# Kernel tuning notes

Measured on AMD Instinct MI355X. Metric: run time of the kernel, lower is better.

The kernel has to match this reference:

```python
import jax, jax.numpy as jnp
import numpy as np

B, N, D, H, DK, DV, R = 4, 256, 256, 8, 32, 32, 64
EPS = 1e-6


def setup_inputs() -> dict:
    key = jax.random.key(0)
    ks = jax.random.split(key, 16)
    s = D ** -0.5
    return {
        "q": jax.random.normal(ks[0], (B, N, D), jnp.float32),
        "k": jax.random.normal(ks[1], (B, N, D), jnp.float32),
        "v": jax.random.normal(ks[2], (B, N, D), jnp.float32),
        "mask": jax.random.randint(ks[3], (B, N, N), 0, 2).astype(jnp.int32),
        "link": jax.random.uniform(ks[4], (B, N, N, R), jnp.float32),
        "Wq": jax.random.normal(ks[5], (D, H * DK), jnp.float32) * s,
        "Wk": jax.random.normal(ks[6], (D, H * DK), jnp.float32) * s,
        "Wr": jax.random.normal(ks[7], (D, H * DK), jnp.float32) * s,
        "Wv": jax.random.normal(ks[8], (D, H * DV), jnp.float32) * s,
        "Wvv": jax.random.normal(ks[9], (D, H * DV), jnp.float32) * s,
        "relationE": jax.random.normal(ks[10], (R, D), jnp.float32) * s,
        "Wo": jax.random.normal(ks[11], (H * DV, D), jnp.float32) * s,
        "gamma": jnp.ones((D,), jnp.float32),
        "beta": jnp.zeros((D,), jnp.float32),
    }


def reference(q, k, v, mask, link, Wq, Wk, Wr, Wv, Wvv, relationE, Wo, gamma, beta):
    # rela_num != 0 branch of Ruleformer MultiHeadAttention (dropout = identity, eval mode).
    residual = q
    b, n, d = q.shape
    # per-head projections of X (== q == residual in this branch): [b,h,n,dk]
    Xq = (q @ Wq).reshape(b, n, H, DK).transpose(0, 2, 1, 3)
    Xk = (q @ Wk).reshape(b, n, H, DK).transpose(0, 2, 1, 3)
    Xv = (q @ Wv).reshape(b, n, H, DV).transpose(0, 2, 1, 3)

    # calcE: relation-biased scores. Rk[b,i,j,h,d] = (link @ relationE @ Wr)
    Rk = jnp.einsum('bijr,re->bije', link, relationE @ Wr).reshape(b, n, n, H, DK)
    # attn[b,h,i,j] = Xq[b,h,i] . (Xk[b,h,j] + Rk[b,i,j,h])
    attn = jnp.einsum('bhid,bhjd->bhij', Xq, Xk)
    attn = attn + jnp.einsum('bijhd,bhid->bhij', Rk, Xq)
    attn = attn / (DK ** 0.5)
    attn = jnp.where(mask[:, None, :, :] == 0, -1e9, attn)
    alpha = jax.nn.softmax(attn, axis=-1)  # [b,h,n,n]

    # calcZ: Z[b,h,i] = sum_j alpha[b,h,i,j] * (Xv[b,h,j] + Rv[b,i,j,h])
    Rv = jnp.einsum('bijr,re->bije', link, relationE @ Wvv).reshape(b, n, n, H, DV)
    Z = jnp.einsum('bhij,bhjd->bhid', alpha, Xv)
    Z = Z + jnp.einsum('bhij,bijhd->bhid', alpha, Rv)

    out = Z.transpose(0, 2, 1, 3).reshape(b, n, H * DV) @ Wo
    out = out + residual
    mu = out.mean(-1, keepdims=True)
    var = ((out - mu) ** 2).mean(-1, keepdims=True)
    out = (out - mu) * jax.lax.rsqrt(var + EPS) * gamma + beta
    return out, alpha
```

## Files before the change

### kernel.cpp

```cpp
#include <hip/hip_runtime.h>
#include <math.h>

constexpr int B_ = 4, N_ = 256, D_ = 256, H_ = 8, DK_ = 32, DV_ = 32, R_ = 64;
constexpr float SCALE_ = 0.17677669529663687f;
constexpr float EPS_ = 1e-6f;

__global__ __launch_bounds__(256) void ekev_kernel(
        const float* __restrict__ relE, const float* __restrict__ Wr,
        const float* __restrict__ Wvv, float* __restrict__ Ek,
        float* __restrict__ Ev) {
    int r = blockIdx.x & 63;
    int which = blockIdx.x >> 6;
    const float* W = which ? Wvv : Wr;
    float* out = which ? Ev : Ek;
    __shared__ float row[256];
    int tid = threadIdx.x;
    row[tid] = relE[r * 256 + tid];
    __syncthreads();
    float acc = 0.f;
    for (int d = 0; d < 256; ++d) acc += row[d] * W[d * 256 + tid];
    out[r * 256 + tid] = acc;
}

__global__ __launch_bounds__(256) void mcat_kernel(
        const float* __restrict__ Wq, const float* __restrict__ Ek,
        float* __restrict__ M) {
    int d = blockIdx.x;
    int t = threadIdx.x;
    __shared__ float wrow[256];
    wrow[t] = Wq[d * 256 + t];
    __syncthreads();
    for (int hr = t; hr < 512; hr += 256) {
        int h = hr >> 6, r = hr & 63;
        const float4* ek4 = (const float4*)(Ek + r * 256 + h * 32);
        const float4* w4 = (const float4*)(wrow + h * 32);
        float acc = 0.f;
#pragma unroll
        for (int k = 0; k < 8; ++k) {
            float4 e = ek4[k], w = w4[k];
            acc += e.x * w.x + e.y * w.y + e.z * w.z + e.w * w.w;
        }
        M[d * 512 + hr] = acc;
    }
}

__global__ __launch_bounds__(256) void projT_kernel(
        const float* __restrict__ q, const float* __restrict__ Wq,
        const float* __restrict__ Wk, const float* __restrict__ Wv,
        const float* __restrict__ M, float* __restrict__ Xq,
        float* __restrict__ Xk, float* __restrict__ Xv,
        float* __restrict__ T) {
    int ct = blockIdx.x >> 4, rt = blockIdx.x & 15;
    int t = threadIdx.x;
    __shared__ float ash[32 * 65];
    __shared__ float bsh[32 * 64];
    const float* W;
    int ncols, cbase;
    if (ct < 4)       { W = Wq; cbase = ct * 64;        ncols = 256; }
    else if (ct < 8)  { W = Wk; cbase = (ct - 4) * 64;  ncols = 256; }
    else if (ct < 12) { W = Wv; cbase = (ct - 8) * 64;  ncols = 256; }
    else              { W = M;  cbase = (ct - 12) * 64; ncols = 512; }
    int ti = t >> 4, tj = t & 15;
    float acc[4][4] = {{0.f}};
    for (int kc = 0; kc < 8; ++kc) {
        __syncthreads();
#pragma unroll
        for (int kk = 0; kk < 2; ++kk) {
            int m = t + kk * 256;
            int i = m >> 3, kq = m & 7;
            float4 v = *(const float4*)(q + (size_t)(rt * 64 + i) * 256 + kc * 32 + kq * 4);
            ash[(kq * 4 + 0) * 65 + i] = v.x;
            ash[(kq * 4 + 1) * 65 + i] = v.y;
            ash[(kq * 4 + 2) * 65 + i] = v.z;
            ash[(kq * 4 + 3) * 65 + i] = v.w;
        }
#pragma unroll
        for (int kk = 0; kk < 2; ++kk) {
            int m = t + kk * 256;
            int k = m >> 4, j4 = m & 15;
            float4 v = *(const float4*)(W + (size_t)(kc * 32 + k) * ncols + cbase + j4 * 4);
            *(float4*)(bsh + k * 64 + j4 * 4) = v;
        }
        __syncthreads();
#pragma unroll 8
        for (int k = 0; k < 32; ++k) {
            float4 av = *(const float4*)(ash + k * 65 + ti * 4);
            float4 bv = *(const float4*)(bsh + k * 64 + tj * 4);
            acc[0][0] += av.x * bv.x; acc[0][1] += av.x * bv.y;
            acc[0][2] += av.x * bv.z; acc[0][3] += av.x * bv.w;
            acc[1][0] += av.y * bv.x; acc[1][1] += av.y * bv.y;
            acc[1][2] += av.y * bv.z; acc[1][3] += av.y * bv.w;
            acc[2][0] += av.z * bv.x; acc[2][1] += av.z * bv.y;
            acc[2][2] += av.z * bv.z; acc[2][3] += av.z * bv.w;
            acc[3][0] += av.w * bv.x; acc[3][1] += av.w * bv.y;
            acc[3][2] += av.w * bv.z; acc[3][3] += av.w * bv.w;
        }
    }
    if (ct < 12) {
        float* dst = (ct < 4) ? Xq : (ct < 8) ? Xk : Xv;
        int gcol = (ct & 3) * 64 + tj * 4;
        int h = gcol >> 5, dk = gcol & 31;
#pragma unroll
        for (int a = 0; a < 4; ++a) {
            int row = rt * 64 + ti * 4 + a;
            int bb = row >> 8, n = row & 255;
            *(float4*)(dst + ((size_t)(bb * 8 + h) * 256 + n) * 32 + dk) =
                make_float4(acc[a][0], acc[a][1], acc[a][2], acc[a][3]);
        }
    } else {
        int gcol = (ct - 12) * 64 + tj * 4;
#pragma unroll
        for (int a = 0; a < 4; ++a) {
            int row = rt * 64 + ti * 4 + a;
            *(float4*)(T + (size_t)row * 512 + gcol) =
                make_float4(acc[a][0], acc[a][1], acc[a][2], acc[a][3]);
        }
    }
}

__global__ __launch_bounds__(256) void qk_kernel(
        const float* __restrict__ Xq, const float* __restrict__ Xk,
        float* __restrict__ qk) {
    int x = blockIdx.x;
    int jt = x & 3, it = (x >> 2) & 3, bh = x >> 4;
    int t = threadIdx.x;
    __shared__ float xqsh[32 * 64];
    __shared__ float xksh[32 * 64];
#pragma unroll
    for (int k = 0; k < 2; ++k) {
        int m = t + k * 256;
        int i = m >> 3, dq4 = m & 7;
        float4 v = *(const float4*)(Xq + ((size_t)(bh * 256 + it * 64 + i)) * 32 + dq4 * 4);
        xqsh[(dq4 * 4 + 0) * 64 + i] = v.x;
        xqsh[(dq4 * 4 + 1) * 64 + i] = v.y;
        xqsh[(dq4 * 4 + 2) * 64 + i] = v.z;
        xqsh[(dq4 * 4 + 3) * 64 + i] = v.w;
        float4 u = *(const float4*)(Xk + ((size_t)(bh * 256 + jt * 64 + i)) * 32 + dq4 * 4);
        xksh[(dq4 * 4 + 0) * 64 + i] = u.x;
        xksh[(dq4 * 4 + 1) * 64 + i] = u.y;
        xksh[(dq4 * 4 + 2) * 64 + i] = u.z;
        xksh[(dq4 * 4 + 3) * 64 + i] = u.w;
    }
    __syncthreads();
    int ti = t >> 4, tj = t & 15;
    float acc[4][4] = {{0.f}};
#pragma unroll 8
    for (int dk = 0; dk < 32; ++dk) {
        float4 av = *(const float4*)(xqsh + dk * 64 + ti * 4);
        float4 bv = *(const float4*)(xksh + dk * 64 + tj * 4);
        acc[0][0] += av.x * bv.x; acc[0][1] += av.x * bv.y;
        acc[0][2] += av.x * bv.z; acc[0][3] += av.x * bv.w;
        acc[1][0] += av.y * bv.x; acc[1][1] += av.y * bv.y;
        acc[1][2] += av.y * bv.z; acc[1][3] += av.y * bv.w;
        acc[2][0] += av.z * bv.x; acc[2][1] += av.z * bv.y;
        acc[2][2] += av.z * bv.z; acc[2][3] += av.z * bv.w;
        acc[3][0] += av.w * bv.x; acc[3][1] += av.w * bv.y;
        acc[3][2] += av.w * bv.z; acc[3][3] += av.w * bv.w;
    }
#pragma unroll
    for (int a = 0; a < 4; ++a) {
        int i = it * 64 + ti * 4 + a;
        *(float4*)(qk + ((size_t)(bh * 256 + i)) * 256 + jt * 64 + tj * 4) =
            make_float4(acc[a][0], acc[a][1], acc[a][2], acc[a][3]);
    }
}

__global__ __launch_bounds__(256) void bias_kernel(
        const float* __restrict__ link, const float* __restrict__ T,
        float* __restrict__ biasOut) {
    int x = blockIdx.x;
    int jt = x & 3, bi = x >> 2;
    int b = bi >> 8, i = bi & 255;
    int t = threadIdx.x;
    __shared__ float linksh[64 * 67];
    __shared__ float Tsh[512];
    __shared__ float part[4 * 512];
    Tsh[t] = T[(size_t)bi * 512 + t];
    Tsh[256 + t] = T[(size_t)bi * 512 + 256 + t];
    {
        const float4* lp = (const float4*)(link + ((size_t)(bi * 256 + jt * 64)) * 64);
#pragma unroll
        for (int k = 0; k < 4; ++k) {
            int m = t + k * 256;
            float4 v = lp[m];
            int j = m >> 4, c = (m & 15) * 4;
            float* dst = linksh + j * 67 + c;
            dst[0] = v.x; dst[1] = v.y; dst[2] = v.z; dst[3] = v.w;
        }
    }
    __syncthreads();
    int j = t & 63, rg = t >> 6;
    float pacc[8] = {0.f, 0.f, 0.f, 0.f, 0.f, 0.f, 0.f, 0.f};
    for (int rr = 0; rr < 16; ++rr) {
        int r = rg * 16 + rr;
        float lv = linksh[j * 67 + r];
#pragma unroll
        for (int h = 0; h < 8; ++h) pacc[h] += lv * Tsh[h * 64 + r];
    }
#pragma unroll
    for (int h = 0; h < 8; ++h) part[rg * 512 + h * 64 + j] = pacc[h];
    __syncthreads();
    int hp = t >> 6;
#pragma unroll
    for (int e = 0; e < 2; ++e) {
        int h = hp * 2 + e;
        float sum = part[h * 64 + j] + part[512 + h * 64 + j] +
                    part[1024 + h * 64 + j] + part[1536 + h * 64 + j];
        biasOut[((size_t)(b * 8 + h) * 256 + i) * 256 + jt * 64 + j] = sum;
    }
}

__global__ __launch_bounds__(256) void softmax_kernel(
        const float* __restrict__ qk, const int* __restrict__ mask,
        float* __restrict__ alpha) {
    int bi = blockIdx.x;
    int b = bi >> 8, i = bi & 255;
    int t = threadIdx.x;
    __shared__ float redsh[64];
    int j = t;
    float s[8];
#pragma unroll
    for (int h = 0; h < 8; ++h) {
        size_t off = ((size_t)(b * 8 + h) * 256 + i) * 256 + j;
        s[h] = (qk[off] + alpha[off]) * SCALE_;
    }
    if (mask[(b * 256 + i) * 256 + j] == 0) {
#pragma unroll
        for (int h = 0; h < 8; ++h) s[h] = -1e9f;
    }
    int lane = t & 63, wv = t >> 6;
#pragma unroll
    for (int h = 0; h < 8; ++h) {
        float v = s[h];
        for (int off = 32; off > 0; off >>= 1) v = fmaxf(v, __shfl_xor(v, off));
        if (lane == 0) redsh[h * 4 + wv] = v;
    }
    __syncthreads();
    float mx[8];
#pragma unroll
    for (int h = 0; h < 8; ++h)
        mx[h] = fmaxf(fmaxf(redsh[h * 4 + 0], redsh[h * 4 + 1]),
                      fmaxf(redsh[h * 4 + 2], redsh[h * 4 + 3]));
    __syncthreads();
#pragma unroll
    for (int h = 0; h < 8; ++h) {
        float e = __expf(s[h] - mx[h]);
        s[h] = e;
        float v = e;
        for (int off = 32; off > 0; off >>= 1) v += __shfl_xor(v, off);
        if (lane == 0) redsh[h * 4 + wv] = v;
    }
    __syncthreads();
#pragma unroll
    for (int h = 0; h < 8; ++h) {
        float esum = redsh[h * 4 + 0] + redsh[h * 4 + 1] +
                     redsh[h * 4 + 2] + redsh[h * 4 + 3];
        alpha[((size_t)(b * 8 + h) * 256 + i) * 256 + j] = s[h] * (1.f / esum);
    }
}

__global__ __launch_bounds__(256) void spart_kernel(
        const float* __restrict__ link, const float* __restrict__ alpha,
        float* __restrict__ Spart) {
    int x = blockIdx.x;
    int jt = x & 1, bi = x >> 1;
    int b = bi >> 8, i = bi & 255;
    int t = threadIdx.x;
    __shared__ float linksh[128 * 67];
    __shared__ float ashm[1024];
    __shared__ float part[4 * 512];
    {
        const float4* lp = (const float4*)(link + ((size_t)(bi * 256 + jt * 128)) * 64);
#pragma unroll
        for (int k = 0; k < 8; ++k) {
            int m = t + k * 256;
            float4 v = lp[m];
            int j = m >> 4, c = (m & 15) * 4;
            float* dst = linksh + j * 67 + c;
            dst[0] = v.x; dst[1] = v.y; dst[2] = v.z; dst[3] = v.w;
        }
    }
#pragma unroll
    for (int k = 0; k < 4; ++k) {
        int m = t + k * 256;
        int h = m >> 7, j = m & 127;
        ashm[m] = alpha[((size_t)(b * 8 + h) * 256 + i) * 256 + jt * 128 + j];
    }
    __syncthreads();
    int r = t & 63, jg = t >> 6;
    float pacc[8] = {0.f, 0.f, 0.f, 0.f, 0.f, 0.f, 0.f, 0.f};
    for (int jj = 0; jj < 32; ++jj) {
        int j = jg * 32 + jj;
        float lv = linksh[j * 67 + r];
#pragma unroll
        for (int h = 0; h < 8; ++h) pacc[h] += ashm[h * 128 + j] * lv;
    }
#pragma unroll
    for (int h = 0; h < 8; ++h) part[jg * 512 + h * 64 + r] = pacc[h];
    __syncthreads();
    for (int hr = t; hr < 512; hr += 256) {
        float sum = part[hr] + part[512 + hr] + part[1024 + hr] + part[1536 + hr];
        Spart[(size_t)x * 512 + hr] = sum;
    }
}

__global__ __launch_bounds__(256) void zx_kernel(
        const float* __restrict__ alpha, const float* __restrict__ Xv,
        float* __restrict__ Zx) {
    int x = blockIdx.x;
    int it = x & 7, bh = x >> 3;
    int t = threadIdx.x;
    __shared__ float ashm[32 * 64];
    __shared__ float xvsh[64 * 32];
    int dv = t & 31, ig = t >> 5;
    float acc[4] = {0.f, 0.f, 0.f, 0.f};
    for (int cc = 0; cc < 4; ++cc) {
        __syncthreads();
#pragma unroll
        for (int k = 0; k < 2; ++k) {
            int m = t + k * 256;
            int i = m >> 4, jq = m & 15;
            float4 v = *(const float4*)(alpha + ((size_t)(bh * 256 + it * 32 + i)) * 256 + cc * 64 + jq * 4);
            float* dst = ashm + i * 64 + jq * 4;
            dst[0] = v.x; dst[1] = v.y; dst[2] = v.z; dst[3] = v.w;
            ((float4*)xvsh)[m] = *(const float4*)(Xv + ((size_t)(bh * 256 + cc * 64)) * 32 + m * 4);
        }
        __syncthreads();
        for (int j = 0; j < 64; ++j) {
            float xv = xvsh[j * 32 + dv];
#pragma unroll
            for (int ii = 0; ii < 4; ++ii)
                acc[ii] += ashm[(ig * 4 + ii) * 64 + j] * xv;
        }
    }
#pragma unroll
    for (int ii = 0; ii < 4; ++ii)
        Zx[((size_t)(bh * 256 + it * 32 + ig * 4 + ii)) * 32 + dv] = acc[ii];
}

__global__ __launch_bounds__(256) void outz_kernel(
        const float* __restrict__ Spart, const float* __restrict__ Zx,
        const float* __restrict__ Ev, const float* __restrict__ Wo,
        const float* __restrict__ q, const float* __restrict__ gamma,
        const float* __restrict__ beta, float* __restrict__ out) {
    int blk = blockIdx.x;
    int t = threadIdx.x;
    __shared__ float Ssh[4 * 512];
    __shared__ float zsh[4 * 256];
    __shared__ float redsh[32];
    for (int m = t; m < 2048; m += 256) {
        int rr = m >> 9, hr = m & 511;
        size_t bi = (size_t)(blk * 4 + rr);
        Ssh[m] = Spart[bi * 1024 + hr] + Spart[bi * 1024 + 512 + hr];
    }
    __syncthreads();
    int h = t >> 5, dv = t & 31;
    int row0 = blk * 4;
    int b = row0 >> 8;
    float z[4];
#pragma unroll
    for (int rr = 0; rr < 4; ++rr) {
        int i = (row0 + rr) & 255;
        z[rr] = Zx[((size_t)((b * 8 + h) * 256 + i)) * 32 + dv];
    }
    for (int r = 0; r < 64; ++r) {
        float ev = Ev[r * 256 + h * 32 + dv];
#pragma unroll
        for (int rr = 0; rr < 4; ++rr) z[rr] += Ssh[rr * 512 + h * 64 + r] * ev;
    }
#pragma unroll
    for (int rr = 0; rr < 4; ++rr) zsh[rr * 256 + t] = z[rr];
    __syncthreads();
    float acc[4];
#pragma unroll
    for (int rr = 0; rr < 4; ++rr) acc[rr] = q[(row0 + rr) * 256 + t];
    for (int d4 = 0; d4 < 64; ++d4) {
        float w0 = Wo[(d4 * 4 + 0) * 256 + t];
        float w1 = Wo[(d4 * 4 + 1) * 256 + t];
        float w2 = Wo[(d4 * 4 + 2) * 256 + t];
        float w3 = Wo[(d4 * 4 + 3) * 256 + t];
#pragma unroll
        for (int rr = 0; rr < 4; ++rr) {
            float4 zv = *(const float4*)(zsh + rr * 256 + d4 * 4);
            acc[rr] += zv.x * w0 + zv.y * w1 + zv.z * w2 + zv.w * w3;
        }
    }
    int lane = t & 63, wv = t >> 6;
#pragma unroll
    for (int rr = 0; rr < 4; ++rr) {
        float v = acc[rr], v2 = acc[rr] * acc[rr];
        for (int off = 32; off > 0; off >>= 1) {
            v += __shfl_xor(v, off);
            v2 += __shfl_xor(v2, off);
        }
        if (lane == 0) {
            redsh[rr * 8 + wv] = v;
            redsh[rr * 8 + 4 + wv] = v2;
        }
    }
    __syncthreads();
#pragma unroll
    for (int rr = 0; rr < 4; ++rr) {
        float sum = redsh[rr * 8 + 0] + redsh[rr * 8 + 1] + redsh[rr * 8 + 2] + redsh[rr * 8 + 3];
        float sum2 = redsh[rr * 8 + 4] + redsh[rr * 8 + 5] + redsh[rr * 8 + 6] + redsh[rr * 8 + 7];
        float mu = sum * (1.f / 256.f);
        float var = sum2 * (1.f / 256.f) - mu * mu;
        float dev = acc[rr] - mu;
        out[(row0 + rr) * 256 + t] = dev * rsqrtf(var + EPS_) * gamma[t] + beta[t];
    }
}

extern "C" void kernel_launch(void* const* d_in, const int* in_sizes, int n_in,
                              void* d_out, int out_size, void* d_ws, size_t ws_size,
                              hipStream_t stream) {
    const float* q     = (const float*)d_in[0];
    const int*   mask  = (const int*)d_in[3];
    const float* link  = (const float*)d_in[4];
    const float* Wq    = (const float*)d_in[5];
    const float* Wk    = (const float*)d_in[6];
    const float* Wr    = (const float*)d_in[7];
    const float* Wv    = (const float*)d_in[8];
    const float* Wvv   = (const float*)d_in[9];
    const float* relE  = (const float*)d_in[10];
    const float* Wo    = (const float*)d_in[11];
    const float* gamma = (const float*)d_in[12];
    const float* beta  = (const float*)d_in[13];

    float* out   = (float*)d_out;
    float* alpha = out + B_ * N_ * D_;

    float* ws    = (float*)d_ws;
    float* Ek    = ws;
    float* Ev    = Ek + 16384;
    float* Mcat  = Ev + 16384;
    float* Xq    = Mcat + 131072;
    float* Xk    = Xq + 262144;
    float* Xv    = Xk + 262144;
    float* T     = Xv + 262144;
    float* qkbuf = T + 524288;
    float* Spart = qkbuf + 2097152;
    float* Zx    = Spart + 1048576;

    ekev_kernel<<<128, 256, 0, stream>>>(relE, Wr, Wvv, Ek, Ev);
    mcat_kernel<<<256, 256, 0, stream>>>(Wq, Ek, Mcat);
    projT_kernel<<<320, 256, 0, stream>>>(q, Wq, Wk, Wv, Mcat, Xq, Xk, Xv, T);
    qk_kernel<<<512, 256, 0, stream>>>(Xq, Xk, qkbuf);
    bias_kernel<<<4096, 256, 0, stream>>>(link, T, alpha);
    softmax_kernel<<<1024, 256, 0, stream>>>(qkbuf, mask, alpha);
    spart_kernel<<<2048, 256, 0, stream>>>(link, alpha, Spart);
    zx_kernel<<<256, 256, 0, stream>>>(alpha, Xv, Zx);
    outz_kernel<<<256, 256, 0, stream>>>(Spart, Zx, Ev, Wo, q, gamma, beta, out);
}
```

Baseline: 213.2 us.

## Fuse bias, softmax, link-weighted sum and Zx into one attention kernel

Four kernels (bias, softmax, spart, zx) are merged into a single per-(b,i) kernel that loads the row's link tile into shared memory once and reuses it for the bias and the alpha-weighted relation sum. The Ev projection moves from the output kernel into this fused kernel. This drops the second 64 MB read of link, the round trips of the bias through alpha and of Spart through global memory, and several launches. In exchange each block needs about 66 KB of shared memory and 512 threads, which limits occupancy, and the Xv reads in the Zx part are strided and not coalesced across j.

```diff
diff --git a/kernel.cpp b/kernel.cpp
--- a/kernel.cpp
+++ b/kernel.cpp
@@ -4,6 +4,7 @@
 constexpr int B_ = 4, N_ = 256, D_ = 256, H_ = 8, DK_ = 32, DV_ = 32, R_ = 64;
 constexpr float SCALE_ = 0.17677669529663687f;
 constexpr float EPS_ = 1e-6f;
+constexpr int LST = 65;
 
 __global__ __launch_bounds__(256) void ekev_kernel(
         const float* __restrict__ relE, const float* __restrict__ Wr,
@@ -165,215 +166,165 @@
     }
 }
 
-__global__ __launch_bounds__(256) void bias_kernel(
-        const float* __restrict__ link, const float* __restrict__ T,
-        float* __restrict__ biasOut) {
-    int x = blockIdx.x;
-    int jt = x & 3, bi = x >> 2;
-    int b = bi >> 8, i = bi & 255;
-    int t = threadIdx.x;
-    __shared__ float linksh[64 * 67];
-    __shared__ float Tsh[512];
-    __shared__ float part[4 * 512];
-    Tsh[t] = T[(size_t)bi * 512 + t];
-    Tsh[256 + t] = T[(size_t)bi * 512 + 256 + t];
-    {
-        const float4* lp = (const float4*)(link + ((size_t)(bi * 256 + jt * 64)) * 64);
-#pragma unroll
-        for (int k = 0; k < 4; ++k) {
-            int m = t + k * 256;
-            float4 v = lp[m];
-            int j = m >> 4, c = (m & 15) * 4;
-            float* dst = linksh + j * 67 + c;
-            dst[0] = v.x; dst[1] = v.y; dst[2] = v.z; dst[3] = v.w;
-        }
-    }
-    __syncthreads();
-    int j = t & 63, rg = t >> 6;
-    float pacc[8] = {0.f, 0.f, 0.f, 0.f, 0.f, 0.f, 0.f, 0.f};
-    for (int rr = 0; rr < 16; ++rr) {
-        int r = rg * 16 + rr;
-        float lv = linksh[j * 67 + r];
-#pragma unroll
-        for (int h = 0; h < 8; ++h) pacc[h] += lv * Tsh[h * 64 + r];
-    }
-#pragma unroll
-    for (int h = 0; h < 8; ++h) part[rg * 512 + h * 64 + j] = pacc[h];
-    __syncthreads();
-    int hp = t >> 6;
-#pragma unroll
-    for (int e = 0; e < 2; ++e) {
-        int h = hp * 2 + e;
-        float sum = part[h * 64 + j] + part[512 + h * 64 + j] +
-                    part[1024 + h * 64 + j] + part[1536 + h * 64 + j];
-        biasOut[((size_t)(b * 8 + h) * 256 + i) * 256 + jt * 64 + j] = sum;
-    }
-}
-
-__global__ __launch_bounds__(256) void softmax_kernel(
+__global__ __launch_bounds__(512) void fusedattn_kernel(
+        const float* __restrict__ link, const float* __restrict__ Tg,
         const float* __restrict__ qk, const int* __restrict__ mask,
-        float* __restrict__ alpha) {
+        const float* __restrict__ Xv, const float* __restrict__ Ev,
+        float* __restrict__ alpha, float* __restrict__ Zx) {
     int bi = blockIdx.x;
     int b = bi >> 8, i = bi & 255;
     int t = threadIdx.x;
+    __shared__ float linksh[256 * LST];
+    __shared__ float ashm[2048];
+    __shared__ float part[2048];
+    __shared__ float Tsh[512];
     __shared__ float redsh[64];
-    int j = t;
-    float s[8];
-#pragma unroll
-    for (int h = 0; h < 8; ++h) {
-        size_t off = ((size_t)(b * 8 + h) * 256 + i) * 256 + j;
-        s[h] = (qk[off] + alpha[off]) * SCALE_;
-    }
-    if (mask[(b * 256 + i) * 256 + j] == 0) {
-#pragma unroll
-        for (int h = 0; h < 8; ++h) s[h] = -1e9f;
-    }
-    int lane = t & 63, wv = t >> 6;
-#pragma unroll
-    for (int h = 0; h < 8; ++h) {
-        float v = s[h];
-        for (int off = 32; off > 0; off >>= 1) v = fmaxf(v, __shfl_xor(v, off));
-        if (lane == 0) redsh[h * 4 + wv] = v;
-    }
-    __syncthreads();
-    float mx[8];
-#pragma unroll
-    for (int h = 0; h < 8; ++h)
-        mx[h] = fmaxf(fmaxf(redsh[h * 4 + 0], redsh[h * 4 + 1]),
-                      fmaxf(redsh[h * 4 + 2], redsh[h * 4 + 3]));
-    __syncthreads();
-#pragma unroll
-    for (int h = 0; h < 8; ++h) {
-        float e = __expf(s[h] - mx[h]);
-        s[h] = e;
-        float v = e;
-        for (int off = 32; off > 0; off >>= 1) v += __shfl_xor(v, off);
-        if (lane == 0) redsh[h * 4 + wv] = v;
-    }
-    __syncthreads();
-#pragma unroll
-    for (int h = 0; h < 8; ++h) {
-        float esum = redsh[h * 4 + 0] + redsh[h * 4 + 1] +
-                     redsh[h * 4 + 2] + redsh[h * 4 + 3];
-        alpha[((size_t)(b * 8 + h) * 256 + i) * 256 + j] = s[h] * (1.f / esum);
-    }
-}
-
-__global__ __launch_bounds__(256) void spart_kernel(
-        const float* __restrict__ link, const float* __restrict__ alpha,
-        float* __restrict__ Spart) {
-    int x = blockIdx.x;
-    int jt = x & 1, bi = x >> 1;
-    int b = bi >> 8, i = bi & 255;
-    int t = threadIdx.x;
-    __shared__ float linksh[128 * 67];
-    __shared__ float ashm[1024];
-    __shared__ float part[4 * 512];
+
     {
-        const float4* lp = (const float4*)(link + ((size_t)(bi * 256 + jt * 128)) * 64);
+        const float4* lp = (const float4*)(link + (size_t)bi * 16384);
 #pragma unroll
         for (int k = 0; k < 8; ++k) {
-            int m = t + k * 256;
+            int m = t + k * 512;
             float4 v = lp[m];
             int j = m >> 4, c = (m & 15) * 4;
-            float* dst = linksh + j * 67 + c;
+            float* dst = linksh + j * LST + c;
             dst[0] = v.x; dst[1] = v.y; dst[2] = v.z; dst[3] = v.w;
         }
     }
-#pragma unroll
-    for (int k = 0; k < 4; ++k) {
-        int m = t + k * 256;
-        int h = m >> 7, j = m & 127;
-        ashm[m] = alpha[((size_t)(b * 8 + h) * 256 + i) * 256 + jt * 128 + j];
-    }
-    __syncthreads();
-    int r = t & 63, jg = t >> 6;
+    Tsh[t] = Tg[(size_t)bi * 512 + t];
+    float qkv[8];
+    int mk = 1;
+    if (t < 256) {
+#pragma unroll
+        for (int h = 0; h < 8; ++h)
+            qkv[h] = qk[((size_t)(b * 8 + h) * 256 + i) * 256 + t];
+        mk = mask[(b * 256 + i) * 256 + t];
+    }
+    __syncthreads();
+
     float pacc[8] = {0.f, 0.f, 0.f, 0.f, 0.f, 0.f, 0.f, 0.f};
-    for (int jj = 0; jj < 32; ++jj) {
-        int j = jg * 32 + jj;
-        float lv = linksh[j * 67 + r];
-#pragma unroll
-        for (int h = 0; h < 8; ++h) pacc[h] += ashm[h * 128 + j] * lv;
-    }
-#pragma unroll
-    for (int h = 0; h < 8; ++h) part[jg * 512 + h * 64 + r] = pacc[h];
-    __syncthreads();
-    for (int hr = t; hr < 512; hr += 256) {
-        float sum = part[hr] + part[512 + hr] + part[1024 + hr] + part[1536 + hr];
-        Spart[(size_t)x * 512 + hr] = sum;
-    }
-}
-
-__global__ __launch_bounds__(256) void zx_kernel(
-        const float* __restrict__ alpha, const float* __restrict__ Xv,
-        float* __restrict__ Zx) {
-    int x = blockIdx.x;
-    int it = x & 7, bh = x >> 3;
-    int t = threadIdx.x;
-    __shared__ float ashm[32 * 64];
-    __shared__ float xvsh[64 * 32];
-    int dv = t & 31, ig = t >> 5;
-    float acc[4] = {0.f, 0.f, 0.f, 0.f};
-    for (int cc = 0; cc < 4; ++cc) {
-        __syncthreads();
-#pragma unroll
-        for (int k = 0; k < 2; ++k) {
-            int m = t + k * 256;
-            int i = m >> 4, jq = m & 15;
-            float4 v = *(const float4*)(alpha + ((size_t)(bh * 256 + it * 32 + i)) * 256 + cc * 64 + jq * 4);
-            float* dst = ashm + i * 64 + jq * 4;
-            dst[0] = v.x; dst[1] = v.y; dst[2] = v.z; dst[3] = v.w;
-            ((float4*)xvsh)[m] = *(const float4*)(Xv + ((size_t)(bh * 256 + cc * 64)) * 32 + m * 4);
-        }
-        __syncthreads();
-        for (int j = 0; j < 64; ++j) {
-            float xv = xvsh[j * 32 + dv];
-#pragma unroll
-            for (int ii = 0; ii < 4; ++ii)
-                acc[ii] += ashm[(ig * 4 + ii) * 64 + j] * xv;
-        }
-    }
-#pragma unroll
-    for (int ii = 0; ii < 4; ++ii)
-        Zx[((size_t)(bh * 256 + it * 32 + ig * 4 + ii)) * 32 + dv] = acc[ii];
+    {
+        int j = t & 255, r0 = (t >> 8) * 32;
+#pragma unroll 8
+        for (int rr = 0; rr < 32; ++rr) {
+            int r = r0 + rr;
+            float lv = linksh[j * LST + r];
+#pragma unroll
+            for (int h = 0; h < 8; ++h) pacc[h] += lv * Tsh[h * 64 + r];
+        }
+    }
+    if (t >= 256) {
+        int j = t & 255;
+#pragma unroll
+        for (int h = 0; h < 8; ++h) part[h * 256 + j] = pacc[h];
+    }
+    __syncthreads();
+
+    float s[8];
+    int lane = t & 63, wv = t >> 6;
+    if (t < 256) {
+#pragma unroll
+        for (int h = 0; h < 8; ++h) {
+            float v = (pacc[h] + part[h * 256 + t] + qkv[h]) * SCALE_;
+            s[h] = (mk == 0) ? -1e9f : v;
+            float m = s[h];
+            for (int off = 32; off > 0; off >>= 1) m = fmaxf(m, __shfl_xor(m, off));
+            if (lane == 0) redsh[h * 4 + wv] = m;
+        }
+    }
+    __syncthreads();
+    if (t < 256) {
+#pragma unroll
+        for (int h = 0; h < 8; ++h) {
+            float mx = fmaxf(fmaxf(redsh[h * 4 + 0], redsh[h * 4 + 1]),
+                             fmaxf(redsh[h * 4 + 2], redsh[h * 4 + 3]));
+            float e = __expf(s[h] - mx);
+            s[h] = e;
+            float v = e;
+            for (int off = 32; off > 0; off >>= 1) v += __shfl_xor(v, off);
+            if (lane == 0) redsh[32 + h * 4 + wv] = v;
+        }
+    }
+    __syncthreads();
+    if (t < 256) {
+#pragma unroll
+        for (int h = 0; h < 8; ++h) {
+            float esum = redsh[32 + h * 4 + 0] + redsh[32 + h * 4 + 1] +
+                         redsh[32 + h * 4 + 2] + redsh[32 + h * 4 + 3];
+            float a = s[h] * (1.f / esum);
+            ashm[h * 256 + t] = a;
+            alpha[((size_t)(b * 8 + h) * 256 + i) * 256 + t] = a;
+        }
+    }
+    __syncthreads();
+
+    float pacc2[8] = {0.f, 0.f, 0.f, 0.f, 0.f, 0.f, 0.f, 0.f};
+    int r = t & 63, g = t >> 6;
+    {
+        int j0 = g * 32;
+#pragma unroll 8
+        for (int jj = 0; jj < 32; ++jj) {
+            int j = j0 + jj;
+            float lv = linksh[j * LST + r];
+#pragma unroll
+            for (int h = 0; h < 8; ++h) pacc2[h] += ashm[h * 256 + j] * lv;
+        }
+    }
+    if (g >= 4) {
+#pragma unroll
+        for (int h = 0; h < 8; ++h) part[(g - 4) * 512 + h * 64 + r] = pacc2[h];
+    }
+    __syncthreads();
+    if (g < 4) {
+#pragma unroll
+        for (int h = 0; h < 8; ++h) part[g * 512 + h * 64 + r] += pacc2[h];
+    }
+    __syncthreads();
+    Tsh[t] = part[t] + part[512 + t] + part[1024 + t] + part[1536 + t];
+    __syncthreads();
+
+    {
+        int h = (t >> 5) & 7, dv = t & 31;
+        float z = 0.f;
+        const float* xv = Xv + ((size_t)(b * 8 + h) * 256) * 32 + dv;
+        if (t < 256) {
+#pragma unroll 4
+            for (int j = 0; j < 128; ++j) z += ashm[h * 256 + j] * xv[j * 32];
+        } else {
+#pragma unroll 4
+            for (int j = 128; j < 256; ++j) z += ashm[h * 256 + j] * xv[j * 32];
+            const float* ev = Ev + h * 32 + dv;
+#pragma unroll 4
+            for (int rr = 0; rr < 64; ++rr) z += Tsh[h * 64 + rr] * ev[rr * 256];
+        }
+        part[t] = z;
+    }
+    __syncthreads();
+    if (t < 256) {
+        int h = t >> 5, dv = t & 31;
+        Zx[((size_t)(b * 8 + h) * 256 + i) * 32 + dv] = part[t] + part[256 + t];
+    }
 }
 
 __global__ __launch_bounds__(256) void outz_kernel(
-        const float* __restrict__ Spart, const float* __restrict__ Zx,
-        const float* __restrict__ Ev, const float* __restrict__ Wo,
+        const float* __restrict__ Zx, const float* __restrict__ Wo,
         const float* __restrict__ q, const float* __restrict__ gamma,
         const float* __restrict__ beta, float* __restrict__ out) {
     int blk = blockIdx.x;
     int t = threadIdx.x;
-    __shared__ float Ssh[4 * 512];
     __shared__ float zsh[4 * 256];
     __shared__ float redsh[32];
-    for (int m = t; m < 2048; m += 256) {
-        int rr = m >> 9, hr = m & 511;
-        size_t bi = (size_t)(blk * 4 + rr);
-        Ssh[m] = Spart[bi * 1024 + hr] + Spart[bi * 1024 + 512 + hr];
-    }
-    __syncthreads();
-    int h = t >> 5, dv = t & 31;
-    int row0 = blk * 4;
-    int b = row0 >> 8;
-    float z[4];
-#pragma unroll
-    for (int rr = 0; rr < 4; ++rr) {
-        int i = (row0 + rr) & 255;
-        z[rr] = Zx[((size_t)((b * 8 + h) * 256 + i)) * 32 + dv];
-    }
-    for (int r = 0; r < 64; ++r) {
-        float ev = Ev[r * 256 + h * 32 + dv];
-#pragma unroll
-        for (int rr = 0; rr < 4; ++rr) z[rr] += Ssh[rr * 512 + h * 64 + r] * ev;
-    }
-#pragma unroll
-    for (int rr = 0; rr < 4; ++rr) zsh[rr * 256 + t] = z[rr];
+    for (int m = t; m < 1024; m += 256) {
+        int rr = m >> 8, d = m & 255;
+        int h = d >> 5, dv = d & 31;
+        int bn = blk * 4 + rr;
+        int b = bn >> 8, i = bn & 255;
+        zsh[rr * 256 + d] = Zx[((size_t)(b * 8 + h) * 256 + i) * 32 + dv];
+    }
     __syncthreads();
     float acc[4];
 #pragma unroll
-    for (int rr = 0; rr < 4; ++rr) acc[rr] = q[(row0 + rr) * 256 + t];
+    for (int rr = 0; rr < 4; ++rr) acc[rr] = q[(blk * 4 + rr) * 256 + t];
     for (int d4 = 0; d4 < 64; ++d4) {
         float w0 = Wo[(d4 * 4 + 0) * 256 + t];
         float w1 = Wo[(d4 * 4 + 1) * 256 + t];
@@ -406,7 +357,7 @@
         float mu = sum * (1.f / 256.f);
         float var = sum2 * (1.f / 256.f) - mu * mu;
         float dev = acc[rr] - mu;
-        out[(row0 + rr) * 256 + t] = dev * rsqrtf(var + EPS_) * gamma[t] + beta[t];
+        out[(blk * 4 + rr) * 256 + t] = dev * rsqrtf(var + EPS_) * gamma[t] + beta[t];
     }
 }
 
@@ -438,16 +389,13 @@
     float* Xv    = Xk + 262144;
     float* T     = Xv + 262144;
     float* qkbuf = T + 524288;
-    float* Spart = qkbuf + 2097152;
-    float* Zx    = Spart + 1048576;
+    float* Zx    = qkbuf + 2097152;
 
     ekev_kernel<<<128, 256, 0, stream>>>(relE, Wr, Wvv, Ek, Ev);
     mcat_kernel<<<256, 256, 0, stream>>>(Wq, Ek, Mcat);
     projT_kernel<<<320, 256, 0, stream>>>(q, Wq, Wk, Wv, Mcat, Xq, Xk, Xv, T);
     qk_kernel<<<512, 256, 0, stream>>>(Xq, Xk, qkbuf);
-    bias_kernel<<<4096, 256, 0, stream>>>(link, T, alpha);
-    softmax_kernel<<<1024, 256, 0, stream>>>(qkbuf, mask, alpha);
-    spart_kernel<<<2048, 256, 0, stream>>>(link, alpha, Spart);
-    zx_kernel<<<256, 256, 0, stream>>>(alpha, Xv, Zx);
-    outz_kernel<<<256, 256, 0, stream>>>(Spart, Zx, Ev, Wo, q, gamma, beta, out);
-}
+    fusedattn_kernel<<<1024, 512, 0, stream>>>(link, T, qkbuf, mask, Xv, Ev,
+                                               alpha, Zx);
+    outz_kernel<<<256, 256, 0, stream>>>(Zx, Wo, q, gamma, beta, out);
+}
```

New measurement: 261.9 us. +22.8%, slower.

## Fuse softmax with alpha-weighted link reduction into one kernel

Applied to the files above, without the earlier changes.

Merges the softmax kernel and the spart kernel, so each block computes its alpha row and immediately reduces it against the link rows for that (b,i). The alpha reread from global memory and one kernel launch go away, and the partial S buffer is halved because each block now covers all 256 j and writes a single S row. In exchange, link is read straight from global memory with per-lane strided loads instead of being staged through LDS as float4, and the grid drops from 2048 to 1024 blocks with more shared memory per block.

```diff
diff --git a/kernel.cpp b/kernel.cpp
--- a/kernel.cpp
+++ b/kernel.cpp
@@ -210,13 +210,17 @@
     }
 }
 
-__global__ __launch_bounds__(256) void softmax_kernel(
+__global__ __launch_bounds__(256) void smsp_kernel(
         const float* __restrict__ qk, const int* __restrict__ mask,
-        float* __restrict__ alpha) {
+        const float* __restrict__ link, float* __restrict__ alpha,
+        float* __restrict__ S) {
     int bi = blockIdx.x;
     int b = bi >> 8, i = bi & 255;
     int t = threadIdx.x;
+    __shared__ float ashm[2048];
+    __shared__ float part[2048];
     __shared__ float redsh[64];
+
     int j = t;
     float s[8];
 #pragma unroll
@@ -248,59 +252,40 @@
         s[h] = e;
         float v = e;
         for (int off = 32; off > 0; off >>= 1) v += __shfl_xor(v, off);
-        if (lane == 0) redsh[h * 4 + wv] = v;
+        if (lane == 0) redsh[32 + h * 4 + wv] = v;
     }
     __syncthreads();
 #pragma unroll
     for (int h = 0; h < 8; ++h) {
-        float esum = redsh[h * 4 + 0] + redsh[h * 4 + 1] +
-                     redsh[h * 4 + 2] + redsh[h * 4 + 3];
-        alpha[((size_t)(b * 8 + h) * 256 + i) * 256 + j] = s[h] * (1.f / esum);
-    }
-}
-
-__global__ __launch_bounds__(256) void spart_kernel(
-        const float* __restrict__ link, const float* __restrict__ alpha,
-        float* __restrict__ Spart) {
-    int x = blockIdx.x;
-    int jt = x & 1, bi = x >> 1;
-    int b = bi >> 8, i = bi & 255;
-    int t = threadIdx.x;
-    __shared__ float linksh[128 * 67];
-    __shared__ float ashm[1024];
-    __shared__ float part[4 * 512];
-    {
-        const float4* lp = (const float4*)(link + ((size_t)(bi * 256 + jt * 128)) * 64);
-#pragma unroll
-        for (int k = 0; k < 8; ++k) {
-            int m = t + k * 256;
-            float4 v = lp[m];
-            int j = m >> 4, c = (m & 15) * 4;
-            float* dst = linksh + j * 67 + c;
-            dst[0] = v.x; dst[1] = v.y; dst[2] = v.z; dst[3] = v.w;
-        }
-    }
-#pragma unroll
-    for (int k = 0; k < 4; ++k) {
-        int m = t + k * 256;
-        int h = m >> 7, j = m & 127;
-        ashm[m] = alpha[((size_t)(b * 8 + h) * 256 + i) * 256 + jt * 128 + j];
-    }
-    __syncthreads();
-    int r = t & 63, jg = t >> 6;
+        float esum = redsh[32 + h * 4 + 0] + redsh[32 + h * 4 + 1] +
+                     redsh[32 + h * 4 + 2] + redsh[32 + h * 4 + 3];
+        float a = s[h] * (1.f / esum);
+        ashm[h * 256 + j] = a;
+        alpha[((size_t)(b * 8 + h) * 256 + i) * 256 + j] = a;
+    }
+    __syncthreads();
+
+    int r = t & 63, g = t >> 6;
     float pacc[8] = {0.f, 0.f, 0.f, 0.f, 0.f, 0.f, 0.f, 0.f};
-    for (int jj = 0; jj < 32; ++jj) {
-        int j = jg * 32 + jj;
-        float lv = linksh[j * 67 + r];
-#pragma unroll
-        for (int h = 0; h < 8; ++h) pacc[h] += ashm[h * 128 + j] * lv;
-    }
-#pragma unroll
-    for (int h = 0; h < 8; ++h) part[jg * 512 + h * 64 + r] = pacc[h];
+    const float* lp = link + ((size_t)(bi * 256 + g * 64)) * 64 + r;
+#pragma unroll 4
+    for (int j4 = 0; j4 < 16; ++j4) {
+        float l0 = lp[(j4 * 4 + 0) * 64];
+        float l1 = lp[(j4 * 4 + 1) * 64];
+        float l2 = lp[(j4 * 4 + 2) * 64];
+        float l3 = lp[(j4 * 4 + 3) * 64];
+#pragma unroll
+        for (int h = 0; h < 8; ++h) {
+            float4 a = *(const float4*)(ashm + h * 256 + g * 64 + j4 * 4);
+            pacc[h] += a.x * l0 + a.y * l1 + a.z * l2 + a.w * l3;
+        }
+    }
+#pragma unroll
+    for (int h = 0; h < 8; ++h) part[g * 512 + h * 64 + r] = pacc[h];
     __syncthreads();
     for (int hr = t; hr < 512; hr += 256) {
-        float sum = part[hr] + part[512 + hr] + part[1024 + hr] + part[1536 + hr];
-        Spart[(size_t)x * 512 + hr] = sum;
+        S[(size_t)bi * 512 + hr] =
+            part[hr] + part[512 + hr] + part[1024 + hr] + part[1536 + hr];
     }
 }
 
@@ -339,7 +324,7 @@
 }
 
 __global__ __launch_bounds__(256) void outz_kernel(
-        const float* __restrict__ Spart, const float* __restrict__ Zx,
+        const float* __restrict__ S, const float* __restrict__ Zx,
         const float* __restrict__ Ev, const float* __restrict__ Wo,
         const float* __restrict__ q, const float* __restrict__ gamma,
         const float* __restrict__ beta, float* __restrict__ out) {
@@ -350,8 +335,7 @@
     __shared__ float redsh[32];
     for (int m = t; m < 2048; m += 256) {
         int rr = m >> 9, hr = m & 511;
-        size_t bi = (size_t)(blk * 4 + rr);
-        Ssh[m] = Spart[bi * 1024 + hr] + Spart[bi * 1024 + 512 + hr];
+        Ssh[m] = S[(size_t)(blk * 4 + rr) * 512 + hr];
     }
     __syncthreads();
     int h = t >> 5, dv = t & 31;
@@ -438,16 +422,15 @@
     float* Xv    = Xk + 262144;
     float* T     = Xv + 262144;
     float* qkbuf = T + 524288;
-    float* Spart = qkbuf + 2097152;
-    float* Zx    = Spart + 1048576;
+    float* S     = qkbuf + 2097152;
+    float* Zx    = S + 524288;
 
     ekev_kernel<<<128, 256, 0, stream>>>(relE, Wr, Wvv, Ek, Ev);
     mcat_kernel<<<256, 256, 0, stream>>>(Wq, Ek, Mcat);
     projT_kernel<<<320, 256, 0, stream>>>(q, Wq, Wk, Wv, Mcat, Xq, Xk, Xv, T);
     qk_kernel<<<512, 256, 0, stream>>>(Xq, Xk, qkbuf);
     bias_kernel<<<4096, 256, 0, stream>>>(link, T, alpha);
-    softmax_kernel<<<1024, 256, 0, stream>>>(qkbuf, mask, alpha);
-    spart_kernel<<<2048, 256, 0, stream>>>(link, alpha, Spart);
+    smsp_kernel<<<1024, 256, 0, stream>>>(qkbuf, mask, link, alpha, S);
     zx_kernel<<<256, 256, 0, stream>>>(alpha, Xv, Zx);
-    outz_kernel<<<256, 256, 0, stream>>>(Spart, Zx, Ev, Wo, q, gamma, beta, out);
-}
+    outz_kernel<<<256, 256, 0, stream>>>(S, Zx, Ev, Wo, q, gamma, beta, out);
+}
```

Measured after the change: 208.9 us. -2.0%, faster.
